# Kernel tuning notes

Hardware: AMD Instinct MI355X
Metric: run time of the kernel (lower is better)

The kernel has to match this reference:

```python
import jax, jax.numpy as jnp
import numpy as np

NUM_HEADS = 16
SPARSITY = 0.1


def setup_inputs() -> dict:
    key = jax.random.key(0)
    ks = jax.random.split(key, 11)
    B, S, D = 2, 2048, 1024
    s = 0.02
    return {
        "query": jax.random.normal(ks[0], (B, S, D), jnp.float32),
        "key": jax.random.normal(ks[1], (B, S, D), jnp.float32),
        "value": jax.random.normal(ks[2], (B, S, D), jnp.float32),
        "Wq": jax.random.normal(ks[3], (D, D), jnp.float32) * s,
        "bq": jax.random.normal(ks[4], (D,), jnp.float32) * s,
        "Wk": jax.random.normal(ks[5], (D, D), jnp.float32) * s,
        "bk": jax.random.normal(ks[6], (D,), jnp.float32) * s,
        "Wv": jax.random.normal(ks[7], (D, D), jnp.float32) * s,
        "bv": jax.random.normal(ks[8], (D,), jnp.float32) * s,
        "Wo": jax.random.normal(ks[9], (D, D), jnp.float32) * s,
        "bo": jax.random.normal(ks[10], (D,), jnp.float32) * s,
    }


def reference(query, key, value, Wq, bq, Wk, bk, Wv, bv, Wo, bo):
    B, Q, D = query.shape
    K = key.shape[1]
    H = NUM_HEADS
    hd = D // H
    scale = 1.0 / np.sqrt(hd).astype(np.float32)

    # projections (torch Linear: x @ W^T + b), split heads -> [B,H,len,hd]
    q = (query @ Wq.T + bq).reshape(B, Q, H, hd).transpose(0, 2, 1, 3)
    k = (key @ Wk.T + bk).reshape(B, K, H, hd).transpose(0, 2, 1, 3)
    v = (value @ Wv.T + bv).reshape(B, K, H, hd).transpose(0, 2, 1, 3)

    # dense relevance scores [B,H,Q,K]
    rel = jnp.einsum('bhqd,bhkd->bhqk', q, k) * scale

    # top-k threshold mask (keep scores >= k-th largest per query row)
    k_per_query = max(1, int(K * SPARSITY))
    top_rel = jax.lax.top_k(rel, k_per_query)[0]
    threshold = top_rel[..., -1:]  # [B,H,Q,1]
    attn = jnp.where(rel < threshold, -jnp.inf, rel)
    attn = jax.nn.softmax(attn, axis=-1)

    out = jnp.einsum('bhqk,bhkd->bhqd', attn, v)
    out = out.transpose(0, 2, 1, 3).reshape(B, Q, D)
    return out @ Wo.T + bo
```

## Files before the change

kernel.cpp:

```cpp
#include <hip/hip_runtime.h>
#include <math.h>

#define D_MODEL 1024
#define SEQ     2048
#define NB      2
#define NH      16
#define HD      64
#define BH      (NB*NH)
#define M_TOK   (NB*SEQ)
#define KSEL    204
#define TQ      16
#define LCAP    256
#define CCAP    96
#define KPW     256

typedef __attribute__((ext_vector_type(8))) short bf16x8;
typedef __attribute__((ext_vector_type(4))) float f32x4;
typedef __attribute__((ext_vector_type(4))) unsigned short us4;
typedef __attribute__((ext_vector_type(8))) unsigned short us8;

__device__ __forceinline__ unsigned short f2bf(float x) {
    unsigned u = __float_as_uint(x);
    return (unsigned short)((u + 0x7FFFu + ((u >> 16) & 1u)) >> 16);
}
__device__ __forceinline__ float bf2f(unsigned short h) {
    return __uint_as_float(((unsigned)h) << 16);
}

__device__ __forceinline__ int binOfE(int e) {
    int b = (e + 4194304) >> 15;
    return b < 0 ? 0 : (b > 255 ? 255 : b);
}

__device__ __forceinline__ void gload_lds16(const unsigned short* g,
                                            unsigned short* l) {
    __builtin_amdgcn_global_load_lds(
        (const __attribute__((address_space(1))) unsigned int*)g,
        (__attribute__((address_space(3))) unsigned int*)l, 16, 0, 0);
}

__global__ __launch_bounds__(256) void preconv3_kernel(
    const float* __restrict__ s0, const float* __restrict__ s1,
    const float* __restrict__ s2,
    unsigned short* __restrict__ h0, unsigned short* __restrict__ l0,
    unsigned short* __restrict__ h1, unsigned short* __restrict__ l1,
    unsigned short* __restrict__ h2, unsigned short* __restrict__ l2)
{
    const float* src; unsigned short* hi; unsigned short* lo;
    if (blockIdx.y == 0)      { src = s0; hi = h0; lo = l0; }
    else if (blockIdx.y == 1) { src = s1; hi = h1; lo = l1; }
    else                      { src = s2; hi = h2; lo = l2; }
    int i = (blockIdx.x * 256 + threadIdx.x) * 4;
    float4 v = *(const float4*)(src + i);
    float e[4] = {v.x, v.y, v.z, v.w};
    us4 h, l;
#pragma unroll
    for (int k = 0; k < 4; ++k) {
        unsigned short hh = f2bf(e[k]);
        h[k] = hh; l[k] = f2bf(e[k] - bf2f(hh));
    }
    *(us4*)(hi + i) = h;
    *(us4*)(lo + i) = l;
}

__global__ __launch_bounds__(256) void preconv1_kernel(
    const float* __restrict__ src,
    unsigned short* __restrict__ hi, unsigned short* __restrict__ lo)
{
    int i = (blockIdx.x * 256 + threadIdx.x) * 4;
    float4 v = *(const float4*)(src + i);
    float e[4] = {v.x, v.y, v.z, v.w};
    us4 h, l;
#pragma unroll
    for (int k = 0; k < 4; ++k) {
        unsigned short hh = f2bf(e[k]);
        h[k] = hh; l[k] = f2bf(e[k] - bf2f(hh));
    }
    *(us4*)(hi + i) = h;
    *(us4*)(lo + i) = l;
}

template<int MODE, int TERMS, int AF32>
__device__ __forceinline__ void mfma_gemm_body(
    const float* __restrict__ Xf,
    const unsigned short* __restrict__ XH, const unsigned short* __restrict__ XL,
    const unsigned short* __restrict__ WH, const unsigned short* __restrict__ WL,
    const float* __restrict__ bias,
    float* __restrict__ Cf, unsigned short* __restrict__ Chi,
    unsigned short* __restrict__ Clo, unsigned short* lds)
{
    unsigned short* Ah = lds;
    unsigned short* Al = lds + 4096;
    unsigned short* Bh = lds + 8192;
    unsigned short* Bl = lds + 12288;

    const int tid  = threadIdx.x;
    const int lane = tid & 63;
    const int w    = tid >> 6;
    const int mq   = w & 1;
    const int nq   = w >> 1;
    const int m0   = blockIdx.y * 128;
    const int n0   = blockIdx.x * 128;

    f32x4 acc[4][4];
#pragma unroll
    for (int i = 0; i < 4; ++i)
#pragma unroll
        for (int j = 0; j < 4; ++j) acc[i][j] = (f32x4){0.f, 0.f, 0.f, 0.f};

    for (int k0 = 0; k0 < D_MODEL; k0 += 32) {
        float4 xa[4];
        if (AF32) {
#pragma unroll
            for (int r = 0; r < 4; ++r) {
                int f = tid + 256 * r;
                int row = f >> 3, q4 = f & 7;
                xa[r] = *(const float4*)(Xf + (size_t)(m0 + row) * D_MODEL + k0 + q4 * 4);
            }
        }
        __syncthreads();

#pragma unroll
        for (int r2 = 0; r2 < 2; ++r2) {
            int m = tid + 256 * r2;
            int fi = (m & 0x1C0) | ((m & 15) << 2) | ((m >> 4) & 3);
            int row = fi >> 2, k8 = fi & 3;
            size_t g = (size_t)(n0 + row) * D_MODEL + k0 + k8 * 8;
            int ldsb = (r2 * 256 + (tid & ~63)) * 8;
            gload_lds16(WH + g, Bh + ldsb);
            gload_lds16(WL + g, Bl + ldsb);
        }
        if (AF32) {
#pragma unroll
            for (int r = 0; r < 4; ++r) {
                int f = tid + 256 * r;
                int row = f >> 3, q4 = f & 7;
                int off = (row >> 4) * 512 + ((row & 15) + (q4 >> 1) * 16) * 8 + (q4 & 1) * 4;
                float ax[4] = {xa[r].x, xa[r].y, xa[r].z, xa[r].w};
                us4 ahv, alv;
#pragma unroll
                for (int e = 0; e < 4; ++e) {
                    unsigned short h1 = f2bf(ax[e]);
                    ahv[e] = h1; alv[e] = f2bf(ax[e] - bf2f(h1));
                }
                *(us4*)(Ah + off) = ahv;  *(us4*)(Al + off) = alv;
            }
        } else {
#pragma unroll
            for (int r2 = 0; r2 < 2; ++r2) {
                int m = tid + 256 * r2;
                int fi = (m & 0x1C0) | ((m & 15) << 2) | ((m >> 4) & 3);
                int row = fi >> 2, k8 = fi & 3;
                size_t g = (size_t)(m0 + row) * D_MODEL + k0 + k8 * 8;
                int ldsb = (r2 * 256 + (tid & ~63)) * 8;
                gload_lds16(XH + g, Ah + ldsb);
                gload_lds16(XL + g, Al + ldsb);
            }
        }
        __syncthreads();

        bf16x8 fah[4], fal[4], fbh[4], fbl[4];
#pragma unroll
        for (int i = 0; i < 4; ++i) {
            fah[i] = *(const bf16x8*)(Ah + (mq * 4 + i) * 512 + lane * 8);
            fal[i] = *(const bf16x8*)(Al + (mq * 4 + i) * 512 + lane * 8);
            fbh[i] = *(const bf16x8*)(Bh + (nq * 4 + i) * 512 + lane * 8);
            fbl[i] = *(const bf16x8*)(Bl + (nq * 4 + i) * 512 + lane * 8);
        }
#pragma unroll
        for (int i = 0; i < 4; ++i)
#pragma unroll
            for (int j = 0; j < 4; ++j) {
                acc[i][j] = __builtin_amdgcn_mfma_f32_16x16x32_bf16(fah[i], fbh[j], acc[i][j], 0, 0, 0);
                acc[i][j] = __builtin_amdgcn_mfma_f32_16x16x32_bf16(fah[i], fbl[j], acc[i][j], 0, 0, 0);
                acc[i][j] = __builtin_amdgcn_mfma_f32_16x16x32_bf16(fal[i], fbh[j], acc[i][j], 0, 0, 0);
                if (TERMS == 4)
                    acc[i][j] = __builtin_amdgcn_mfma_f32_16x16x32_bf16(fal[i], fbl[j], acc[i][j], 0, 0, 0);
            }
    }

    const int quad = lane >> 4;
    const int rl   = lane & 15;
#pragma unroll
    for (int jt = 0; jt < 4; ++jt) {
        int n = n0 + nq * 64 + jt * 16 + rl;
        float bn = bias[n];
        int h = n >> 6, dd = n & 63;
#pragma unroll
        for (int it = 0; it < 4; ++it) {
#pragma unroll
            for (int r = 0; r < 4; ++r) {
                int m = m0 + mq * 64 + it * 16 + quad * 4 + r;
                float v = acc[it][jt][r] + bn;
                if (MODE == 0) {
                    Cf[(size_t)m * D_MODEL + n] = v;
                } else {
                    int b = m >> 11, s = m & 2047;
                    size_t o = (size_t)(((b << 4) + h) * SEQ + s) * HD + dd;
                    if (MODE == 1) {
                        Cf[o] = v;
                    } else {
                        unsigned short hi = f2bf(v);
                        Chi[o] = hi;
                        Clo[o] = f2bf(v - bf2f(hi));
                    }
                }
            }
        }
    }
}

__global__ __launch_bounds__(256) void proj_qkv_kernel(
    const float* __restrict__ qin, const float* __restrict__ kin, const float* __restrict__ vin,
    const unsigned short* __restrict__ wqh, const unsigned short* __restrict__ wql,
    const unsigned short* __restrict__ wkh, const unsigned short* __restrict__ wkl,
    const unsigned short* __restrict__ wvh, const unsigned short* __restrict__ wvl,
    const float* __restrict__ bq, const float* __restrict__ bk, const float* __restrict__ bv,
    unsigned short* qhi, unsigned short* qlo,
    unsigned short* khi, unsigned short* klo,
    float* vws)
{
    __shared__ unsigned short lds[16384];
    if (blockIdx.z == 0)
        mfma_gemm_body<2, 4, 1>(qin, nullptr, nullptr, wqh, wql, bq,
                                nullptr, qhi, qlo, lds);
    else if (blockIdx.z == 1)
        mfma_gemm_body<2, 4, 1>(kin, nullptr, nullptr, wkh, wkl, bk,
                                nullptr, khi, klo, lds);
    else
        mfma_gemm_body<1, 3, 1>(vin, nullptr, nullptr, wvh, wvl, bv,
                                vws, nullptr, nullptr, lds);
}

__global__ __launch_bounds__(256) void oproj_kernel(
    const unsigned short* __restrict__ AH, const unsigned short* __restrict__ AL,
    const unsigned short* __restrict__ woh, const unsigned short* __restrict__ wol,
    const float* __restrict__ bo, float* __restrict__ out)
{
    __shared__ unsigned short lds[16384];
    mfma_gemm_body<0, 3, 0>(nullptr, AH, AL, woh, wol, bo,
                            out, nullptr, nullptr, lds);
}

__global__ __launch_bounds__(512, 4) void attn_kernel(
    const unsigned short* __restrict__ qhi, const unsigned short* __restrict__ qlo,
    const unsigned short* __restrict__ khi, const unsigned short* __restrict__ klo,
    const float* __restrict__ vws,
    unsigned short* __restrict__ awsHi, unsigned short* __restrict__ awsLo)
{
    __shared__ union __align__(16) UU {
        int hist[TQ][260];
        struct {
            int2  L[TQ][LCAP];
            float cand[TQ][CCAP];
        } p;
    } u;
    __shared__ float thrv[TQ];
    __shared__ int   kneedS[TQ];
    __shared__ int   sbinS[TQ];
    __shared__ int   candCnt[TQ];
    __shared__ int   cnt[TQ];

    const int tid  = threadIdx.x;
    const int lane = tid & 63;
    const int w    = tid >> 6;
    const int quad = lane >> 4;
    const int rl   = lane & 15;
    const int flat = blockIdx.x;
    const int bh   = (flat & 7) * 4 + ((flat >> 3) & 3);
    const int q0   = (flat >> 5) * TQ;
    const size_t hb = (size_t)bh * SEQ * HD;

    {
        int* hp = &u.hist[0][0];
        for (int i = tid; i < TQ * 260; i += 512) hp[i] = 0;
        if (tid < TQ) { candCnt[tid] = 0; cnt[tid] = 0; }
    }

    const size_t qoff = hb + (size_t)(q0 + rl) * HD + quad * 8;
    bf16x8 bqh0 = *(const bf16x8*)(qhi + qoff);
    bf16x8 bql0 = *(const bf16x8*)(qlo + qoff);
    bf16x8 bqh1 = *(const bf16x8*)(qhi + qoff + 32);
    bf16x8 bql1 = *(const bf16x8*)(qlo + qoff + 32);

    const int kbase = w * KPW;
    __syncthreads();

    unsigned scp[48];
#pragma unroll
    for (int t = 0; t < 16; ++t) {
        const size_t koff = hb + (size_t)(kbase + t * 16 + rl) * HD + quad * 8;
        bf16x8 ah0 = *(const bf16x8*)(khi + koff);
        bf16x8 al0 = *(const bf16x8*)(klo + koff);
        bf16x8 ah1 = *(const bf16x8*)(khi + koff + 32);
        bf16x8 al1 = *(const bf16x8*)(klo + koff + 32);
        f32x4 d0 = {0.f, 0.f, 0.f, 0.f};
        f32x4 d1 = {0.f, 0.f, 0.f, 0.f};
        d0 = __builtin_amdgcn_mfma_f32_16x16x32_bf16(ah0, bqh0, d0, 0, 0, 0);
        d1 = __builtin_amdgcn_mfma_f32_16x16x32_bf16(ah1, bqh1, d1, 0, 0, 0);
        d0 = __builtin_amdgcn_mfma_f32_16x16x32_bf16(ah0, bql0, d0, 0, 0, 0);
        d1 = __builtin_amdgcn_mfma_f32_16x16x32_bf16(ah1, bql1, d1, 0, 0, 0);
        d0 = __builtin_amdgcn_mfma_f32_16x16x32_bf16(al0, bqh0, d0, 0, 0, 0);
        d1 = __builtin_amdgcn_mfma_f32_16x16x32_bf16(al1, bqh1, d1, 0, 0, 0);
        f32x4 d = d0 + d1;
        int e[4];
#pragma unroll
        for (int r = 0; r < 4; ++r) {
            e[r] = (int)__builtin_rintf(d[r] * 262144.f);
            atomicAdd(&u.hist[rl][binOfE(e[r])], 1);
        }
        scp[3*t+0] = ((unsigned)e[0] & 0xFFFFFFu) | ((unsigned)e[1] << 24);
        scp[3*t+1] = (((unsigned)e[1] >> 8) & 0xFFFFu) | ((unsigned)e[2] << 16);
        scp[3*t+2] = (((unsigned)e[2] >> 16) & 0xFFu) | ((unsigned)e[3] << 8);
    }
    __syncthreads();

#pragma unroll
    for (int half = 0; half < 2; ++half) {
        int r = w + half * 8;
        int4 hv = *(const int4*)&u.hist[r][4 * lane];
        int h0 = hv.x, h1 = hv.y, h2 = hv.z, h3 = hv.w;
        int s3 = h3, s2 = h2 + s3, s1 = h1 + s2, s0 = h0 + s1;
        int acc = s0;
#pragma unroll
        for (int off = 1; off < 64; off <<= 1) {
            int v = __shfl_down(acc, off);
            acc += (lane + off < 64) ? v : 0;
        }
        int ehi = acc - s0;
        int suf0 = ehi + s0, suf1 = ehi + s1, suf2 = ehi + s2, suf3 = ehi + s3;
        int selbin = -1, newkn = 0;
        if      (suf3 >= KSEL) { selbin = 4*lane + 3; newkn = KSEL - (suf3 - h3); }
        else if (suf2 >= KSEL) { selbin = 4*lane + 2; newkn = KSEL - (suf2 - h2); }
        else if (suf1 >= KSEL) { selbin = 4*lane + 1; newkn = KSEL - (suf1 - h1); }
        else if (suf0 >= KSEL) { selbin = 4*lane + 0; newkn = KSEL - (suf0 - h0); }
        int pack = ((selbin + 1) << 16) | (newkn & 0xFFFF);
#pragma unroll
        for (int off = 32; off; off >>= 1) {
            int o = __shfl_xor(pack, off);
            pack = pack > o ? pack : o;
        }
        if (lane == 0) {
            sbinS[r]  = (pack >> 16) - 1;
            kneedS[r] = pack & 0xFFFF;
        }
    }
    __syncthreads();

    {
        const int sb = sbinS[rl];
#pragma unroll
        for (int t = 0; t < 16; ++t) {
            unsigned p0 = scp[3*t+0], p1 = scp[3*t+1], p2 = scp[3*t+2];
            int e[4];
            e[0] = ((int)(p0 << 8)) >> 8;
            e[1] = ((int)(((p1 << 8) | (p0 >> 24)) << 8)) >> 8;
            e[2] = ((int)(((p2 << 16) | (p1 >> 16)) << 8)) >> 8;
            e[3] = ((int)p2) >> 8;
#pragma unroll
            for (int r = 0; r < 4; ++r) {
                int b = binOfE(e[r]);
                if (b >= sb) {
                    float dv = (float)e[r] * (1.f / 262144.f);
                    int key = kbase + t * 16 + quad * 4 + r;
                    int pos = atomicAdd(&cnt[rl], 1);
                    if (pos < LCAP)
                        u.p.L[rl][pos] = make_int2(key, __float_as_int(dv));
                    if (b == sb) {
                        int cp = atomicAdd(&candCnt[rl], 1);
                        if (cp < CCAP) u.p.cand[rl][cp] = dv;
                    }
                }
            }
        }
    }
    __syncthreads();

#pragma unroll
    for (int half = 0; half < 2; ++half) {
        int r = w + half * 8;
        int n = candCnt[r]; if (n > CCAP) n = CCAP;
        int kn = kneedS[r];
        bool  a0 = lane < n, a1 = lane + 64 < n;
        float x0 = a0 ? u.p.cand[r][lane]      : 0.f;
        float x1 = a1 ? u.p.cand[r][lane + 64] : 0.f;
        int g0 = 0, e0 = 0, g1 = 0, e1 = 0;
        for (int j = 0; j < n; ++j) {
            float c = u.p.cand[r][j];
            g0 += (c > x0);  e0 += (c == x0);
            g1 += (c > x1);  e1 += (c == x1);
        }
        float best = -1e30f;
        if (a0 && g0 < kn && g0 + e0 >= kn) best = x0;
        if (a1 && g1 < kn && g1 + e1 >= kn) best = best > x1 ? best : x1;
#pragma unroll
        for (int off = 32; off; off >>= 1) {
            float o = __shfl_xor(best, off);
            best = best > o ? best : o;
        }
        if (lane == 0) thrv[r] = best;
    }
    __syncthreads();

    {
        const int b = bh >> 4, h = bh & 15;
        const int slot = lane >> 4;
        const int d16  = lane & 15;
        const float* Vp = vws + hb + d16 * 4;

        const int r0 = w, r1 = w + 8;
        int n0 = cnt[r0]; if (n0 > LCAP) n0 = LCAP;
        int n1 = cnt[r1]; if (n1 > LCAP) n1 = LCAP;
        const float t0 = thrv[r0], t1 = thrv[r1];
        const int nmax = n0 > n1 ? n0 : n1;
        f32x4 a0 = {0.f,0.f,0.f,0.f}, a1 = {0.f,0.f,0.f,0.f};
        float z0 = 0.f, z1 = 0.f;

        for (int j = 0; j < nmax; j += 8) {
            int ia = j + slot, ib = j + 4 + slot;
            int i0a = ia < n0 ? ia : 0,  i0b = ib < n0 ? ib : 0;
            int i1a = ia < n1 ? ia : 0,  i1b = ib < n1 ? ib : 0;
            int2 p0a = u.p.L[r0][i0a];
            int2 p0b = u.p.L[r0][i0b];
            int2 p1a = u.p.L[r1][i1a];
            int2 p1b = u.p.L[r1][i1b];
            float s0a = __int_as_float(p0a.y), s0b = __int_as_float(p0b.y);
            float s1a = __int_as_float(p1a.y), s1b = __int_as_float(p1b.y);
            float w0a = ((ia < n0) && (s0a >= t0))
                        ? __builtin_amdgcn_exp2f((s0a - t0) * 0.1803368801f) : 0.f;
            float w0b = ((ib < n0) && (s0b >= t0))
                        ? __builtin_amdgcn_exp2f((s0b - t0) * 0.1803368801f) : 0.f;
            float w1a = ((ia < n1) && (s1a >= t1))
                        ? __builtin_amdgcn_exp2f((s1a - t1) * 0.1803368801f) : 0.f;
            float w1b = ((ib < n1) && (s1b >= t1))
                        ? __builtin_amdgcn_exp2f((s1b - t1) * 0.1803368801f) : 0.f;
            float4 v0a = *(const float4*)(Vp + (size_t)p0a.x * HD);
            float4 v0b = *(const float4*)(Vp + (size_t)p0b.x * HD);
            float4 v1a = *(const float4*)(Vp + (size_t)p1a.x * HD);
            float4 v1b = *(const float4*)(Vp + (size_t)p1b.x * HD);
            a0[0] += w0a * v0a.x + w0b * v0b.x;
            a0[1] += w0a * v0a.y + w0b * v0b.y;
            a0[2] += w0a * v0a.z + w0b * v0b.z;
            a0[3] += w0a * v0a.w + w0b * v0b.w;
            a1[0] += w1a * v1a.x + w1b * v1b.x;
            a1[1] += w1a * v1a.y + w1b * v1b.y;
            a1[2] += w1a * v1a.z + w1b * v1b.z;
            a1[3] += w1a * v1a.w + w1b * v1b.w;
            z0 += w0a + w0b; z1 += w1a + w1b;
        }
#pragma unroll
        for (int off = 16; off < 64; off <<= 1) {
            a0[0] += __shfl_xor(a0[0], off); a0[1] += __shfl_xor(a0[1], off);
            a0[2] += __shfl_xor(a0[2], off); a0[3] += __shfl_xor(a0[3], off);
            a1[0] += __shfl_xor(a1[0], off); a1[1] += __shfl_xor(a1[1], off);
            a1[2] += __shfl_xor(a1[2], off); a1[3] += __shfl_xor(a1[3], off);
            z0 += __shfl_xor(z0, off);       z1 += __shfl_xor(z1, off);
        }
        if (slot == 0) {
            float zr0 = 1.f / z0, zr1 = 1.f / z1;
            float o0[4] = {a0[0]*zr0, a0[1]*zr0, a0[2]*zr0, a0[3]*zr0};
            float o1[4] = {a1[0]*zr1, a1[1]*zr1, a1[2]*zr1, a1[3]*zr1};
            size_t off0 = ((size_t)(b * SEQ) + q0 + r0) * D_MODEL + h * HD + d16 * 4;
            size_t off1 = ((size_t)(b * SEQ) + q0 + r1) * D_MODEL + h * HD + d16 * 4;
            us4 h0, l0, h1, l1;
#pragma unroll
            for (int e = 0; e < 4; ++e) {
                unsigned short hh0 = f2bf(o0[e]);
                h0[e] = hh0; l0[e] = f2bf(o0[e] - bf2f(hh0));
                unsigned short hh1 = f2bf(o1[e]);
                h1[e] = hh1; l1[e] = f2bf(o1[e] - bf2f(hh1));
            }
            *(us4*)(awsHi + off0) = h0;  *(us4*)(awsLo + off0) = l0;
            *(us4*)(awsHi + off1) = h1;  *(us4*)(awsLo + off1) = l1;
        }
    }
}

extern "C" void kernel_launch(void* const* d_in, const int* in_sizes, int n_in,
                              void* d_out, int out_size, void* d_ws, size_t ws_size,
                              hipStream_t stream)
{
    const float* query = (const float*)d_in[0];
    const float* key   = (const float*)d_in[1];
    const float* value = (const float*)d_in[2];
    const float* Wq    = (const float*)d_in[3];
    const float* bq    = (const float*)d_in[4];
    const float* Wk    = (const float*)d_in[5];
    const float* bk    = (const float*)d_in[6];
    const float* Wv    = (const float*)d_in[7];
    const float* bv    = (const float*)d_in[8];
    const float* Wo    = (const float*)d_in[9];
    const float* bo    = (const float*)d_in[10];
    float* out = (float*)d_out;

    char* wsb = (char*)d_ws;
    const size_t MB = 1024u * 1024u;
    unsigned short* qhi = (unsigned short*)(wsb);
    unsigned short* qlo = (unsigned short*)(wsb + 8 * MB);
    unsigned short* khi = (unsigned short*)(wsb + 16 * MB);
    unsigned short* klo = (unsigned short*)(wsb + 24 * MB);
    float* vws          = (float*)(wsb + 32 * MB);
    unsigned short* wqh = (unsigned short*)(wsb + 48 * MB);
    unsigned short* wql = (unsigned short*)(wsb + 50 * MB);
    unsigned short* wkh = (unsigned short*)(wsb + 52 * MB);
    unsigned short* wkl = (unsigned short*)(wsb + 54 * MB);
    unsigned short* wvh = (unsigned short*)(wsb + 56 * MB);
    unsigned short* wvl = (unsigned short*)(wsb + 58 * MB);
    unsigned short* awsHi = (unsigned short*)(wsb + 48 * MB);
    unsigned short* awsLo = (unsigned short*)(wsb + 56 * MB);
    unsigned short* woh = (unsigned short*)(wsb);
    unsigned short* wol = (unsigned short*)(wsb + 2 * MB);

    preconv3_kernel<<<dim3(1024, 3), 256, 0, stream>>>(
        Wq, Wk, Wv, wqh, wql, wkh, wkl, wvh, wvl);

    dim3 g1(D_MODEL / 128, M_TOK / 128, 3);
    proj_qkv_kernel<<<g1, 256, 0, stream>>>(query, key, value,
                                            wqh, wql, wkh, wkl, wvh, wvl,
                                            bq, bk, bv,
                                            qhi, qlo, khi, klo, vws);

    dim3 g2((SEQ / TQ) * BH);
    attn_kernel<<<g2, 512, 0, stream>>>(qhi, qlo, khi, klo, vws, awsHi, awsLo);

    preconv1_kernel<<<1024, 256, 0, stream>>>(Wo, woh, wol);

    dim3 g3(D_MODEL / 128, M_TOK / 128);
    oproj_kernel<<<g3, 256, 0, stream>>>(awsHi, awsLo, woh, wol, bo, out);
}
```

Measured before the change: 732.9 us.

## Double-buffer LDS tiles in projection GEMMs to overlap loads with MFMA

The shared GEMM body used by the QKV and output projections now keeps two LDS buffers. While MFMAs run on the current tile, it issues the next tile's global-to-LDS copies and f32 A loads, and writes the converted A split only after compute finishes. This removes one barrier per k-step and hides global load latency behind math. LDS per block doubles to 64 KB, which may reduce occupancy.

```diff
diff --git a/kernel.cpp b/kernel.cpp
--- a/kernel.cpp
+++ b/kernel.cpp
@@ -89,11 +89,6 @@
     float* __restrict__ Cf, unsigned short* __restrict__ Chi,
     unsigned short* __restrict__ Clo, unsigned short* lds)
 {
-    unsigned short* Ah = lds;
-    unsigned short* Al = lds + 4096;
-    unsigned short* Bh = lds + 8192;
-    unsigned short* Bl = lds + 12288;
-
     const int tid  = threadIdx.x;
     const int lane = tid & 63;
     const int w    = tid >> 6;
@@ -102,24 +97,7 @@
     const int m0   = blockIdx.y * 128;
     const int n0   = blockIdx.x * 128;
 
-    f32x4 acc[4][4];
-#pragma unroll
-    for (int i = 0; i < 4; ++i)
-#pragma unroll
-        for (int j = 0; j < 4; ++j) acc[i][j] = (f32x4){0.f, 0.f, 0.f, 0.f};
-
-    for (int k0 = 0; k0 < D_MODEL; k0 += 32) {
-        float4 xa[4];
-        if (AF32) {
-#pragma unroll
-            for (int r = 0; r < 4; ++r) {
-                int f = tid + 256 * r;
-                int row = f >> 3, q4 = f & 7;
-                xa[r] = *(const float4*)(Xf + (size_t)(m0 + row) * D_MODEL + k0 + q4 * 4);
-            }
-        }
-        __syncthreads();
-
+    auto stageB = [&](int buf, int k0) {
 #pragma unroll
         for (int r2 = 0; r2 < 2; ++r2) {
             int m = tid + 256 * r2;
@@ -127,38 +105,75 @@
             int row = fi >> 2, k8 = fi & 3;
             size_t g = (size_t)(n0 + row) * D_MODEL + k0 + k8 * 8;
             int ldsb = (r2 * 256 + (tid & ~63)) * 8;
-            gload_lds16(WH + g, Bh + ldsb);
-            gload_lds16(WL + g, Bl + ldsb);
-        }
-        if (AF32) {
-#pragma unroll
-            for (int r = 0; r < 4; ++r) {
-                int f = tid + 256 * r;
-                int row = f >> 3, q4 = f & 7;
-                int off = (row >> 4) * 512 + ((row & 15) + (q4 >> 1) * 16) * 8 + (q4 & 1) * 4;
-                float ax[4] = {xa[r].x, xa[r].y, xa[r].z, xa[r].w};
-                us4 ahv, alv;
-#pragma unroll
-                for (int e = 0; e < 4; ++e) {
-                    unsigned short h1 = f2bf(ax[e]);
-                    ahv[e] = h1; alv[e] = f2bf(ax[e] - bf2f(h1));
-                }
-                *(us4*)(Ah + off) = ahv;  *(us4*)(Al + off) = alv;
+            gload_lds16(WH + g, lds + buf * 16384 + 8192 + ldsb);
+            gload_lds16(WL + g, lds + buf * 16384 + 12288 + ldsb);
+        }
+    };
+    auto stageAcopy = [&](int buf, int k0) {
+#pragma unroll
+        for (int r2 = 0; r2 < 2; ++r2) {
+            int m = tid + 256 * r2;
+            int fi = (m & 0x1C0) | ((m & 15) << 2) | ((m >> 4) & 3);
+            int row = fi >> 2, k8 = fi & 3;
+            size_t g = (size_t)(m0 + row) * D_MODEL + k0 + k8 * 8;
+            int ldsb = (r2 * 256 + (tid & ~63)) * 8;
+            gload_lds16(XH + g, lds + buf * 16384 + ldsb);
+            gload_lds16(XL + g, lds + buf * 16384 + 4096 + ldsb);
+        }
+    };
+    auto loadA = [&](int k0, float4* xa) {
+#pragma unroll
+        for (int r = 0; r < 4; ++r) {
+            int f = tid + 256 * r;
+            int row = f >> 3, q4 = f & 7;
+            xa[r] = *(const float4*)(Xf + (size_t)(m0 + row) * D_MODEL + k0 + q4 * 4);
+        }
+    };
+    auto writeA = [&](int buf, const float4* xa) {
+        unsigned short* Ah = lds + buf * 16384;
+        unsigned short* Al = Ah + 4096;
+#pragma unroll
+        for (int r = 0; r < 4; ++r) {
+            int f = tid + 256 * r;
+            int row = f >> 3, q4 = f & 7;
+            int off = (row >> 4) * 512 + ((row & 15) + (q4 >> 1) * 16) * 8 + (q4 & 1) * 4;
+            float ax[4] = {xa[r].x, xa[r].y, xa[r].z, xa[r].w};
+            us4 ahv, alv;
+#pragma unroll
+            for (int e = 0; e < 4; ++e) {
+                unsigned short h1 = f2bf(ax[e]);
+                ahv[e] = h1; alv[e] = f2bf(ax[e] - bf2f(h1));
             }
-        } else {
-#pragma unroll
-            for (int r2 = 0; r2 < 2; ++r2) {
-                int m = tid + 256 * r2;
-                int fi = (m & 0x1C0) | ((m & 15) << 2) | ((m >> 4) & 3);
-                int row = fi >> 2, k8 = fi & 3;
-                size_t g = (size_t)(m0 + row) * D_MODEL + k0 + k8 * 8;
-                int ldsb = (r2 * 256 + (tid & ~63)) * 8;
-                gload_lds16(XH + g, Ah + ldsb);
-                gload_lds16(XL + g, Al + ldsb);
-            }
-        }
-        __syncthreads();
-
+            *(us4*)(Ah + off) = ahv;  *(us4*)(Al + off) = alv;
+        }
+    };
+
+    f32x4 acc[4][4];
+#pragma unroll
+    for (int i = 0; i < 4; ++i)
+#pragma unroll
+        for (int j = 0; j < 4; ++j) acc[i][j] = (f32x4){0.f, 0.f, 0.f, 0.f};
+
+    float4 xa[4];
+    if (AF32) loadA(0, xa);
+    stageB(0, 0);
+    if (!AF32) stageAcopy(0, 0);
+    if (AF32) writeA(0, xa);
+    __syncthreads();
+
+    int cur = 0;
+    for (int k0 = 0; k0 < D_MODEL; k0 += 32) {
+        const bool hasNext = (k0 + 32) < D_MODEL;
+        if (hasNext) {
+            if (AF32) loadA(k0 + 32, xa);
+            stageB(cur ^ 1, k0 + 32);
+            if (!AF32) stageAcopy(cur ^ 1, k0 + 32);
+        }
+
+        unsigned short* Ah = lds + cur * 16384;
+        unsigned short* Al = Ah + 4096;
+        unsigned short* Bh = Ah + 8192;
+        unsigned short* Bl = Ah + 12288;
         bf16x8 fah[4], fal[4], fbh[4], fbl[4];
 #pragma unroll
         for (int i = 0; i < 4; ++i) {
@@ -177,6 +192,10 @@
                 if (TERMS == 4)
                     acc[i][j] = __builtin_amdgcn_mfma_f32_16x16x32_bf16(fal[i], fbl[j], acc[i][j], 0, 0, 0);
             }
+
+        if (hasNext && AF32) writeA(cur ^ 1, xa);
+        __syncthreads();
+        cur ^= 1;
     }
 
     const int quad = lane >> 4;
@@ -220,7 +239,7 @@
     unsigned short* khi, unsigned short* klo,
     float* vws)
 {
-    __shared__ unsigned short lds[16384];
+    __shared__ unsigned short lds[32768];
     if (blockIdx.z == 0)
         mfma_gemm_body<2, 4, 1>(qin, nullptr, nullptr, wqh, wql, bq,
                                 nullptr, qhi, qlo, lds);
@@ -237,7 +256,7 @@
     const unsigned short* __restrict__ woh, const unsigned short* __restrict__ wol,
     const float* __restrict__ bo, float* __restrict__ out)
 {
-    __shared__ unsigned short lds[16384];
+    __shared__ unsigned short lds[32768];
     mfma_gemm_body<0, 3, 0>(nullptr, AH, AL, woh, wol, bo,
                             out, nullptr, nullptr, lds);
 }
```

After: 694.5 us. 5.2% less time.
